# Performance work log

Measured on AMD Instinct MI355X. Metric: run time of the kernel, lower is better.

The kernel has to match this reference:

```python
import jax, jax.numpy as jnp
import numpy as np
from jax.ops import segment_sum

N_PFAS, N_GW, N_SW = 50000, 200000, 20000
D_IN, D_OUT, D_EDGE = 32, 32, 3
E_PG, E_GP, E_PS, E_SP = 2000000, 2000000, 1000000, 1000000


def _params(key):
    ks = jax.random.split(key, 24)
    g = lambda k, s: jax.random.normal(k, s, dtype=jnp.float32) * 0.05
    p = {}
    # SAGEConvWithEdgeAttr for pg (pfas->gw) and gp (gw->pfas)
    for i, rel in enumerate(['pg', 'gp']):
        o = i * 5
        p[f'Wl_{rel}'] = g(ks[o + 0], (D_IN, D_OUT))
        p[f'bl_{rel}'] = g(ks[o + 1], (D_OUT,))
        p[f'Wr_{rel}'] = g(ks[o + 2], (D_IN, D_OUT))
        p[f'We_{rel}'] = g(ks[o + 3], (D_EDGE, D_OUT))
        p[f'be_{rel}'] = g(ks[o + 4], (D_OUT,))
    # plain SAGEConv for ps (pfas->sw) and sp (sw->pfas)
    for i, rel in enumerate(['ps', 'sp']):
        o = 10 + i * 3
        p[f'Wl_{rel}'] = g(ks[o + 0], (D_IN, D_OUT))
        p[f'bl_{rel}'] = g(ks[o + 1], (D_OUT,))
        p[f'Wr_{rel}'] = g(ks[o + 2], (D_IN, D_OUT))
    p['W_out'] = g(ks[16], (D_OUT, 1))
    p['b_out'] = g(ks[17], (1,))
    p['a_prelu'] = jnp.float32(0.25) * jnp.ones((1,), jnp.float32)
    return p


def setup_inputs() -> dict:
    key = jax.random.key(0)
    ks = jax.random.split(key, 16)
    inp = {
        'x_pfas': jax.random.normal(ks[0], (N_PFAS, D_IN), jnp.float32),
        'x_gw': jax.random.normal(ks[1], (N_GW, D_IN), jnp.float32),
        'x_sw': jax.random.normal(ks[2], (N_SW, D_IN), jnp.float32),
        'src_pg': jax.random.randint(ks[3], (E_PG,), 0, N_PFAS),
        'dst_pg': jax.random.randint(ks[4], (E_PG,), 0, N_GW),
        'ea_pg': jax.random.uniform(ks[5], (E_PG, D_EDGE), jnp.float32),
        'src_gp': jax.random.randint(ks[6], (E_GP,), 0, N_GW),
        'dst_gp': jax.random.randint(ks[7], (E_GP,), 0, N_PFAS),
        'ea_gp': jax.random.uniform(ks[8], (E_GP, D_EDGE), jnp.float32),
        'src_ps': jax.random.randint(ks[9], (E_PS,), 0, N_PFAS),
        'dst_ps': jax.random.randint(ks[10], (E_PS,), 0, N_SW),
        'src_sp': jax.random.randint(ks[11], (E_SP,), 0, N_SW),
        'dst_sp': jax.random.randint(ks[12], (E_SP,), 0, N_PFAS),
    }
    inp.update(_params(ks[13]))
    return inp


def _sage(x_src, x_dst, src, dst, Wl, bl, Wr, n_dst):
    # PyG SAGEConv: lin_l(mean_aggr(x_j)) + lin_r(x_dst); lin_r has no bias
    msg = x_src[src]                                   # [E, D_IN]
    s = segment_sum(msg, dst, num_segments=n_dst)      # [n_dst, D_IN]
    cnt = segment_sum(jnp.ones((src.shape[0],), x_src.dtype), dst, num_segments=n_dst)
    mean = s / jnp.maximum(cnt, 1.0)[:, None]
    return mean @ Wl + bl + x_dst @ Wr


def _edge_scatter_set(dst, ea_t, n_dst):
    # matches torch zeros.scatter_(0, col, edge_attr_transformed): overwrite at dst
    return jnp.zeros((n_dst, ea_t.shape[1]), ea_t.dtype).at[dst].set(ea_t)


def reference(x_pfas, x_gw, x_sw,
              src_pg, dst_pg, ea_pg,
              src_gp, dst_gp, ea_gp,
              src_ps, dst_ps, src_sp, dst_sp,
              Wl_pg, bl_pg, Wr_pg, We_pg, be_pg,
              Wl_gp, bl_gp, Wr_gp, We_gp, be_gp,
              Wl_ps, bl_ps, Wr_ps,
              Wl_sp, bl_sp, Wr_sp,
              W_out, b_out, a_prelu):
    # pfas -> gw (edge attrs)
    out_gw = _sage(x_pfas, x_gw, src_pg, dst_pg, Wl_pg, bl_pg, Wr_pg, N_GW)
    out_gw = out_gw + _edge_scatter_set(dst_pg, ea_pg @ We_pg + be_pg, N_GW)
    # gw -> pfas (edge attrs)
    out_pf1 = _sage(x_gw, x_pfas, src_gp, dst_gp, Wl_gp, bl_gp, Wr_gp, N_PFAS)
    out_pf1 = out_pf1 + _edge_scatter_set(dst_gp, ea_gp @ We_gp + be_gp, N_PFAS)
    # sw -> pfas (plain SAGE)
    out_pf2 = _sage(x_sw, x_pfas, src_sp, dst_sp, Wl_sp, bl_sp, Wr_sp, N_PFAS)
    # pfas -> sw (plain SAGE)
    out_sw = _sage(x_pfas, x_sw, src_ps, dst_ps, Wl_ps, bl_ps, Wr_ps, N_SW)
    # HeteroConv aggr='sum' over relations with same dst type, then relu
    h_pfas = jax.nn.relu(out_pf1 + out_pf2)
    h_gw = jax.nn.relu(out_gw)
    h_sw = jax.nn.relu(out_sw)
    # final linear + PReLU on gw_wells
    y = h_gw @ W_out + b_out                           # [N_GW, 1]
    y = jnp.where(y >= 0, y, a_prelu * y)
    return h_pfas, y, h_sw
```

## Files before the change

kernel.cpp:

```cpp
#include <hip/hip_runtime.h>

typedef unsigned int u32;

#define NPFAS 50000
#define NGW   200000
#define NSW   20000
#define D     32
#define EPG   2000000
#define EGP   2000000
#define EPS   1000000
#define ESP   1000000

#define NB_PG 782
#define NB_GP 782
#define NB_SP 391
#define NB_PS 313
#define CAP_PG 2880
#define CAP_GP 2880
#define CAP_SP 2880
#define CAP_PS 3584
#define SORT_MAX 3584
#define EIDM 0x1FFFFFu

#define ZGCUR    0
#define MAXE_PG  2304
#define MAXE_GP  202304
#define S_PG     252304
#define S_GP     6652304
#define S_SP     8252304
#define S_PS     9852304
#define CNT_PG   10492304
#define CNT_GP   10692304
#define CNT_SP   10742304
#define CNT_PS   10792304
#define REG_PG   10812304
#define REG_GP   13064464
#define REG_SP   15316624
#define REG_PS   16442704

__device__ __forceinline__ void part4(
    const int* __restrict__ src, const int* __restrict__ dst,
    int e0, int e1, int nb, int cp, int cf, int pshift, int bbits, int roundSz,
    bool useEid,
    u32* __restrict__ region, int cap, int* __restrict__ gcur,
    u32* binData, u32* binCnt)
{
    u32 dlm = (1u << bbits) - 1u;
    for (int b = threadIdx.x; b < nb; b += 256) binCnt[b] = 0;
    __syncthreads();
    for (int base = e0; base < e1; base += roundSz) {
        int rend = base + roundSz; if (rend > e1) rend = e1;
        for (int e = base + (int)threadIdx.x; e < rend; e += 256) {
            int d = dst[e];
            int bk = d >> bbits;
            u32 payload = useEid ? (u32)e : (u32)src[e];
            u32 w0 = payload | (((u32)d & dlm) << pshift);
            u32 pos = atomicAdd(&binCnt[bk], 1u);
            if ((int)pos < cp) {
                binData[bk * cp + (int)pos] = w0;
            } else {
                int g = atomicAdd(&gcur[bk], 1);
                if (g < cap) region[(size_t)bk * cap + g] = w0;
            }
        }
        __syncthreads();
        bool last = (base + roundSz >= e1);
        for (int b = threadIdx.x; b < nb; b += 256) {
            int c = (int)binCnt[b];
            if (c > cp) c = cp;
            if (c >= cf || (last && c > 0)) {
                int g = atomicAdd(&gcur[b], c);
                int lim = cap - g; if (lim < 0) lim = 0; if (c > lim) c = lim;
                u32* dp = region + ((size_t)b * cap + g);
                for (int i = 0; i < c; i++) dp[i] = binData[b * cp + i];
                binCnt[b] = 0;
            }
        }
        __syncthreads();
    }
}

__global__ __launch_bounds__(256) void partition_all(
    const int* __restrict__ dst_pg,
    const int* __restrict__ dst_gp,
    const int* __restrict__ src_sp, const int* __restrict__ dst_sp,
    const int* __restrict__ src_ps, const int* __restrict__ dst_ps,
    int* __restrict__ wsi)
{
    __shared__ u32 binData[6256];
    __shared__ u32 binCnt[782];
    u32* ws = (u32*)wsi;
    int b = blockIdx.x;
    if (b < 160) {
        int e0 = b * (EPG / 160);
        part4(nullptr, dst_pg, e0, e0 + EPG / 160, NB_PG, 8, 4, 21, 8, 1024, true,
              ws + REG_PG, CAP_PG, wsi + ZGCUR + 0, binData, binCnt);
    } else if (b < 320) {
        int bb = b - 160;
        int e0 = bb * (EGP / 160);
        part4(nullptr, dst_gp, e0, e0 + EGP / 160, NB_GP, 8, 4, 21, 6, 1024, true,
              ws + REG_GP, CAP_GP, wsi + ZGCUR + 782, binData, binCnt);
    } else if (b < 416) {
        int bb = b - 320;
        int e0 = (int)(((long long)bb * ESP) / 96);
        int e1 = (int)(((long long)(bb + 1) * ESP) / 96);
        part4(src_sp, dst_sp, e0, e1, NB_SP, 16, 8, 15, 7, 1024, false,
              ws + REG_SP, CAP_SP, wsi + ZGCUR + 1564, binData, binCnt);
    } else {
        int bb = b - 416;
        int e0 = (int)(((long long)bb * EPS) / 96);
        int e1 = (int)(((long long)(bb + 1) * EPS) / 96);
        part4(src_ps, dst_ps, e0, e1, NB_PS, 16, 8, 16, 6, 1024, false,
              ws + REG_PS, CAP_PS, wsi + ZGCUR + 1955, binData, binCnt);
    }
}

__global__ __launch_bounds__(256) void sort_agg(
    const float* __restrict__ x_pfas, const float* __restrict__ x_gw,
    const float* __restrict__ x_sw,
    const int* __restrict__ src_pg, const int* __restrict__ src_gp,
    int* __restrict__ wsi)
{
    __shared__ u32 sortedS[SORT_MAX];
    __shared__ int histS[256];
    __shared__ int startS[256];
    __shared__ int cursorS[256];
    __shared__ int mxS[256];
    __shared__ int wsum[4];

    float* wsf = (float*)wsi;
    u32* wsu = (u32*)wsi;
    int tid = threadIdx.x;
    int bid = blockIdx.x;

    const float* x; const u32* reg; const int* srcArr; int gi, cap, pshift, nbDst, dbase, ndst;
    u32 smask; bool useEid; float* sOut; float* cntOut; int* mxOut;

    if (bid < NB_PG) {
        x = x_pfas; reg = wsu + REG_PG + (size_t)bid * CAP_PG; gi = ZGCUR + bid;
        cap = CAP_PG; pshift = 21; smask = 0; useEid = true; srcArr = src_pg;
        nbDst = 256; dbase = bid << 8; ndst = NGW;
        sOut = wsf + S_PG; cntOut = wsf + CNT_PG; mxOut = wsi + MAXE_PG;
    } else if (bid < NB_PG + NB_GP) {
        int b = bid - NB_PG;
        x = x_gw; reg = wsu + REG_GP + (size_t)b * CAP_GP; gi = ZGCUR + 782 + b;
        cap = CAP_GP; pshift = 21; smask = 0; useEid = true; srcArr = src_gp;
        nbDst = 64; dbase = b << 6; ndst = NPFAS;
        sOut = wsf + S_GP; cntOut = wsf + CNT_GP; mxOut = wsi + MAXE_GP;
    } else if (bid < NB_PG + NB_GP + NB_SP) {
        int b = bid - NB_PG - NB_GP;
        x = x_sw; reg = wsu + REG_SP + (size_t)b * CAP_SP; gi = ZGCUR + 1564 + b;
        cap = CAP_SP; pshift = 15; smask = 0x7FFFu; useEid = false; srcArr = nullptr;
        nbDst = 128; dbase = b << 7; ndst = NPFAS;
        sOut = wsf + S_SP; cntOut = wsf + CNT_SP; mxOut = nullptr;
    } else {
        int b = bid - NB_PG - NB_GP - NB_SP;
        x = x_pfas; reg = wsu + REG_PS + (size_t)b * CAP_PS; gi = ZGCUR + 1955 + b;
        cap = CAP_PS; pshift = 16; smask = 0xFFFFu; useEid = false; srcArr = nullptr;
        nbDst = 64; dbase = b << 6; ndst = NSW;
        sOut = wsf + S_PS; cntOut = wsf + CNT_PS; mxOut = nullptr;
    }

    int nEnt = wsi[gi]; if (nEnt > cap) nEnt = cap;

    histS[tid] = 0;
    mxS[tid] = -1;
    __syncthreads();

    for (int i = tid; i < nEnt; i += 256) {
        u32 w0 = reg[i];
        int dl = (int)((w0 >> pshift) & 255u);
        atomicAdd(&histS[dl], 1);
        if (useEid) atomicMax(&mxS[dl], (int)(w0 & EIDM));
    }
    __syncthreads();

    {
        int v = histS[tid];
        int lane = tid & 63, w = tid >> 6;
        int incl = v;
#pragma unroll
        for (int off = 1; off < 64; off <<= 1) {
            int t = __shfl_up(incl, off);
            if (lane >= off) incl += t;
        }
        if (lane == 63) wsum[w] = incl;
        startS[tid] = incl - v;
    }
    __syncthreads();
    {
        int w = tid >> 6;
        int off = 0;
        for (int k = 0; k < w; k++) off += wsum[k];
        int st = startS[tid] + off;
        startS[tid] = st;
        cursorS[tid] = st;
    }
    __syncthreads();

    for (int i = tid; i < nEnt; i += 256) {
        u32 w0 = reg[i];
        int dl = (int)((w0 >> pshift) & 255u);
        int pos = atomicAdd(&cursorS[dl], 1);
        u32 sv = useEid ? (u32)srcArr[(int)(w0 & EIDM)] : (w0 & smask);
        if (pos < SORT_MAX) sortedS[pos] = sv;
    }
    __syncthreads();

    int wv = tid >> 6, lane = tid & 63, half = lane >> 5, f = lane & 31;
    for (int q = wv; q < nbDst; q += 4) {
        int dn = dbase + q;
        if (dn >= ndst) continue;
        int deg = histS[q];
        int p0 = startS[q];
        float a = 0.f;
        int i = half;
        for (; i + 6 < deg; i += 8) {
            int s0 = (int)sortedS[p0 + i];
            int s1 = (int)sortedS[p0 + i + 2];
            int s2 = (int)sortedS[p0 + i + 4];
            int s3 = (int)sortedS[p0 + i + 6];
            float v0 = x[(size_t)s0 * D + f];
            float v1 = x[(size_t)s1 * D + f];
            float v2 = x[(size_t)s2 * D + f];
            float v3 = x[(size_t)s3 * D + f];
            a += (v0 + v1) + (v2 + v3);
        }
        for (; i < deg; i += 2) a += x[(size_t)sortedS[p0 + i] * D + f];
        a += __shfl_xor(a, 32);
        if (half == 0) sOut[(size_t)dn * D + f] = a;
        if (lane == 0) {
            cntOut[dn] = (float)deg;
            if (useEid) mxOut[dn] = mxS[q];
        }
    }
}

__global__ __launch_bounds__(256) void finalize_gw(
    const float* __restrict__ s, const float* __restrict__ cntF,
    const int* __restrict__ maxe,
    const float* __restrict__ x_gw,
    const float* __restrict__ ea,
    const float* __restrict__ Wl, const float* __restrict__ bl,
    const float* __restrict__ Wr, const float* __restrict__ We,
    const float* __restrict__ be,
    const float* __restrict__ W_out, const float* __restrict__ b_out,
    const float* __restrict__ a_prelu,
    float* __restrict__ y_out)
{
    __shared__ __align__(16) float WlT[D * D];
    __shared__ __align__(16) float WrT[D * D];
    __shared__ float WeT[3 * D];
    __shared__ float blS[D], beS[D], WoS[D];
    for (int i = threadIdx.x; i < D * D; i += blockDim.x) {
        int k = i / D, j = i % D;
        WlT[j * D + k] = Wl[i];
        WrT[j * D + k] = Wr[i];
    }
    for (int i = threadIdx.x; i < 3 * D; i += blockDim.x) {
        int k = i / D, j = i % D;
        WeT[j * 3 + k] = We[i];
    }
    if (threadIdx.x < D) {
        blS[threadIdx.x] = bl[threadIdx.x];
        beS[threadIdx.x] = be[threadIdx.x];
        WoS[threadIdx.x] = W_out[threadIdx.x];
    }
    __syncthreads();

    int n = blockIdx.x * blockDim.x + threadIdx.x;
    if (n >= NGW) return;

    float mean[D], xd[D];
    float inv = 1.0f / fmaxf(cntF[n], 1.0f);
    const float4* sp = (const float4*)(s + (size_t)n * D);
    const float4* xp = (const float4*)(x_gw + (size_t)n * D);
#pragma unroll
    for (int q = 0; q < D / 4; q++) {
        float4 sv = sp[q];
        mean[4*q+0] = sv.x * inv; mean[4*q+1] = sv.y * inv;
        mean[4*q+2] = sv.z * inv; mean[4*q+3] = sv.w * inv;
        float4 xv = xp[q];
        xd[4*q+0] = xv.x; xd[4*q+1] = xv.y; xd[4*q+2] = xv.z; xd[4*q+3] = xv.w;
    }
    int me = maxe[n];
    bool he = (me >= 0);
    float e0 = 0.f, e1 = 0.f, e2 = 0.f;
    if (he) {
        e0 = ea[(size_t)me * 3 + 0];
        e1 = ea[(size_t)me * 3 + 1];
        e2 = ea[(size_t)me * 3 + 2];
    }
    float yacc = 0.f;
    for (int j = 0; j < D; j++) {
        float o = blS[j] + (he ? beS[j] : 0.0f);
        const float4* wl4 = (const float4*)(WlT + j * D);
        const float4* wr4 = (const float4*)(WrT + j * D);
#pragma unroll
        for (int q = 0; q < D / 4; q++) {
            float4 wl = wl4[q], wr = wr4[q];
            o += mean[4*q+0]*wl.x + mean[4*q+1]*wl.y + mean[4*q+2]*wl.z + mean[4*q+3]*wl.w;
            o += xd[4*q+0]*wr.x + xd[4*q+1]*wr.y + xd[4*q+2]*wr.z + xd[4*q+3]*wr.w;
        }
        if (he) o += e0*WeT[j*3+0] + e1*WeT[j*3+1] + e2*WeT[j*3+2];
        float h = fmaxf(o, 0.0f);
        yacc += h * WoS[j];
    }
    float y = yacc + b_out[0];
    float ap = a_prelu[0];
    y_out[n] = (y >= 0.f) ? y : ap * y;
}

__global__ __launch_bounds__(256) void finalize_pfas(
    const float* __restrict__ s_gp, const float* __restrict__ cnt_gp,
    const int* __restrict__ maxe_gp,
    const float* __restrict__ s_sp, const float* __restrict__ cnt_sp,
    const float* __restrict__ x_pfas,
    const float* __restrict__ ea,
    const float* __restrict__ Wl_gp, const float* __restrict__ bl_gp,
    const float* __restrict__ Wr_gp, const float* __restrict__ We_gp,
    const float* __restrict__ be_gp,
    const float* __restrict__ Wl_sp, const float* __restrict__ bl_sp,
    const float* __restrict__ Wr_sp,
    float* __restrict__ h_out)
{
    __shared__ __align__(16) float WlgT[D * D];
    __shared__ __align__(16) float WlsT[D * D];
    __shared__ __align__(16) float WrcT[D * D];
    __shared__ float WeT[3 * D];
    __shared__ float blc[D], beS[D];
    for (int i = threadIdx.x; i < D * D; i += blockDim.x) {
        int k = i / D, j = i % D;
        WlgT[j * D + k] = Wl_gp[i];
        WlsT[j * D + k] = Wl_sp[i];
        WrcT[j * D + k] = Wr_gp[i] + Wr_sp[i];
    }
    for (int i = threadIdx.x; i < 3 * D; i += blockDim.x) {
        int k = i / D, j = i % D;
        WeT[j * 3 + k] = We_gp[i];
    }
    if (threadIdx.x < D) {
        blc[threadIdx.x] = bl_gp[threadIdx.x] + bl_sp[threadIdx.x];
        beS[threadIdx.x] = be_gp[threadIdx.x];
    }
    __syncthreads();

    int n = blockIdx.x * blockDim.x + threadIdx.x;
    if (n >= NPFAS) return;

    float mg[D], ms[D], xd[D];
    float invg = 1.0f / fmaxf(cnt_gp[n], 1.0f);
    float invs = 1.0f / fmaxf(cnt_sp[n], 1.0f);
    const float4* gp4 = (const float4*)(s_gp + (size_t)n * D);
    const float4* sp4 = (const float4*)(s_sp + (size_t)n * D);
    const float4* xp4 = (const float4*)(x_pfas + (size_t)n * D);
#pragma unroll
    for (int q = 0; q < D / 4; q++) {
        float4 a = gp4[q];
        mg[4*q+0] = a.x * invg; mg[4*q+1] = a.y * invg; mg[4*q+2] = a.z * invg; mg[4*q+3] = a.w * invg;
        float4 b = sp4[q];
        ms[4*q+0] = b.x * invs; ms[4*q+1] = b.y * invs; ms[4*q+2] = b.z * invs; ms[4*q+3] = b.w * invs;
        float4 c = xp4[q];
        xd[4*q+0] = c.x; xd[4*q+1] = c.y; xd[4*q+2] = c.z; xd[4*q+3] = c.w;
    }
    int me = maxe_gp[n];
    bool he = (me >= 0);
    float e0 = 0.f, e1 = 0.f, e2 = 0.f;
    if (he) {
        e0 = ea[(size_t)me * 3 + 0];
        e1 = ea[(size_t)me * 3 + 1];
        e2 = ea[(size_t)me * 3 + 2];
    }
    float* out = h_out + (size_t)n * D;
    for (int j = 0; j < D; j++) {
        float o = blc[j] + (he ? beS[j] : 0.0f);
        const float4* wg4 = (const float4*)(WlgT + j * D);
        const float4* ws4 = (const float4*)(WlsT + j * D);
        const float4* wc4 = (const float4*)(WrcT + j * D);
#pragma unroll
        for (int q = 0; q < D / 4; q++) {
            float4 wg = wg4[q], wsv = ws4[q], wc = wc4[q];
            o += mg[4*q+0]*wg.x + mg[4*q+1]*wg.y + mg[4*q+2]*wg.z + mg[4*q+3]*wg.w;
            o += ms[4*q+0]*wsv.x + ms[4*q+1]*wsv.y + ms[4*q+2]*wsv.z + ms[4*q+3]*wsv.w;
            o += xd[4*q+0]*wc.x + xd[4*q+1]*wc.y + xd[4*q+2]*wc.z + xd[4*q+3]*wc.w;
        }
        if (he) o += e0*WeT[j*3+0] + e1*WeT[j*3+1] + e2*WeT[j*3+2];
        out[j] = fmaxf(o, 0.0f);
    }
}

__global__ __launch_bounds__(256) void finalize_sw(
    const float* __restrict__ s, const float* __restrict__ cntF,
    const float* __restrict__ x_sw,
    const float* __restrict__ Wl, const float* __restrict__ bl,
    const float* __restrict__ Wr,
    float* __restrict__ h_out)
{
    __shared__ __align__(16) float WlT[D * D];
    __shared__ __align__(16) float WrT[D * D];
    __shared__ float blS[D];
    for (int i = threadIdx.x; i < D * D; i += blockDim.x) {
        int k = i / D, j = i % D;
        WlT[j * D + k] = Wl[i];
        WrT[j * D + k] = Wr[i];
    }
    if (threadIdx.x < D) blS[threadIdx.x] = bl[threadIdx.x];
    __syncthreads();

    int n = blockIdx.x * blockDim.x + threadIdx.x;
    if (n >= NSW) return;

    float mean[D], xd[D];
    float inv = 1.0f / fmaxf(cntF[n], 1.0f);
    const float4* sp = (const float4*)(s + (size_t)n * D);
    const float4* xp = (const float4*)(x_sw + (size_t)n * D);
#pragma unroll
    for (int q = 0; q < D / 4; q++) {
        float4 sv = sp[q];
        mean[4*q+0] = sv.x * inv; mean[4*q+1] = sv.y * inv;
        mean[4*q+2] = sv.z * inv; mean[4*q+3] = sv.w * inv;
        float4 xv = xp[q];
        xd[4*q+0] = xv.x; xd[4*q+1] = xv.y; xd[4*q+2] = xv.z; xd[4*q+3] = xv.w;
    }
    float* out = h_out + (size_t)n * D;
    for (int j = 0; j < D; j++) {
        float o = blS[j];
        const float4* wl4 = (const float4*)(WlT + j * D);
        const float4* wr4 = (const float4*)(WrT + j * D);
#pragma unroll
        for (int q = 0; q < D / 4; q++) {
            float4 wl = wl4[q], wr = wr4[q];
            o += mean[4*q+0]*wl.x + mean[4*q+1]*wl.y + mean[4*q+2]*wl.z + mean[4*q+3]*wl.w;
            o += xd[4*q+0]*wr.x + xd[4*q+1]*wr.y + xd[4*q+2]*wr.z + xd[4*q+3]*wr.w;
        }
        out[j] = fmaxf(o, 0.0f);
    }
}

extern "C" void kernel_launch(void* const* d_in, const int* in_sizes, int n_in,
                              void* d_out, int out_size, void* d_ws, size_t ws_size,
                              hipStream_t stream) {
    (void)in_sizes; (void)n_in; (void)out_size; (void)ws_size;
    const float* x_pfas = (const float*)d_in[0];
    const float* x_gw   = (const float*)d_in[1];
    const float* x_sw   = (const float*)d_in[2];
    const int*   src_pg = (const int*)d_in[3];
    const int*   dst_pg = (const int*)d_in[4];
    const float* ea_pg  = (const float*)d_in[5];
    const int*   src_gp = (const int*)d_in[6];
    const int*   dst_gp = (const int*)d_in[7];
    const float* ea_gp  = (const float*)d_in[8];
    const int*   src_ps = (const int*)d_in[9];
    const int*   dst_ps = (const int*)d_in[10];
    const int*   src_sp = (const int*)d_in[11];
    const int*   dst_sp = (const int*)d_in[12];
    const float* Wl_pg = (const float*)d_in[13];
    const float* bl_pg = (const float*)d_in[14];
    const float* Wr_pg = (const float*)d_in[15];
    const float* We_pg = (const float*)d_in[16];
    const float* be_pg = (const float*)d_in[17];
    const float* Wl_gp = (const float*)d_in[18];
    const float* bl_gp = (const float*)d_in[19];
    const float* Wr_gp = (const float*)d_in[20];
    const float* We_gp = (const float*)d_in[21];
    const float* be_gp = (const float*)d_in[22];
    const float* Wl_ps = (const float*)d_in[23];
    const float* bl_ps = (const float*)d_in[24];
    const float* Wr_ps = (const float*)d_in[25];
    const float* Wl_sp = (const float*)d_in[26];
    const float* bl_sp = (const float*)d_in[27];
    const float* Wr_sp = (const float*)d_in[28];
    const float* W_out = (const float*)d_in[29];
    const float* b_out = (const float*)d_in[30];
    const float* a_pre = (const float*)d_in[31];

    int*   wsi = (int*)d_ws;
    float* wsf = (float*)d_ws;

    hipMemsetAsync(wsi + ZGCUR, 0, 2304 * sizeof(int), stream);

    partition_all<<<512, 256, 0, stream>>>(dst_pg, dst_gp,
                                           src_sp, dst_sp, src_ps, dst_ps, wsi);

    sort_agg<<<NB_PG + NB_GP + NB_SP + NB_PS, 256, 0, stream>>>(
        x_pfas, x_gw, x_sw, src_pg, src_gp, wsi);

    float* out    = (float*)d_out;
    float* h_pfas = out;
    float* y_out  = out + 1600000;
    float* h_sw   = out + 1800000;

    finalize_pfas<<<(NPFAS + 255) / 256, 256, 0, stream>>>(
        wsf + S_GP, wsf + CNT_GP, wsi + MAXE_GP, wsf + S_SP, wsf + CNT_SP,
        x_pfas, ea_gp,
        Wl_gp, bl_gp, Wr_gp, We_gp, be_gp,
        Wl_sp, bl_sp, Wr_sp, h_pfas);

    finalize_gw<<<(NGW + 255) / 256, 256, 0, stream>>>(
        wsf + S_PG, wsf + CNT_PG, wsi + MAXE_PG, x_gw, ea_pg,
        Wl_pg, bl_pg, Wr_pg, We_pg, be_pg,
        W_out, b_out, a_pre, y_out);

    finalize_sw<<<(NSW + 255) / 256, 256, 0, stream>>>(
        wsf + S_PS, wsf + CNT_PS, x_sw, Wl_ps, bl_ps, Wr_ps, h_sw);
}
```

Measured before the change: 511.1 us.

## Gather pfas/gw features from fp16 copies and enlarge partition bin buffers

Adds a kernel that converts x_pfas and x_gw to half precision in workspace, and the neighbor-sum gather in sort_agg reads these fp16 copies to halve gather bytes per edge. The partition kernel also doubles the per-bin shared staging capacity and flush thresholds, so global flushes are fewer and larger. The cost is an extra conversion pass over about 8M floats, fp16 rounding in the aggregated features, and more shared memory per block, which may lower occupancy.

```diff
diff --git a/kernel.cpp b/kernel.cpp
--- a/kernel.cpp
+++ b/kernel.cpp
@@ -1,4 +1,5 @@
 #include <hip/hip_runtime.h>
+#include <hip/hip_fp16.h>
 
 typedef unsigned int u32;
 
@@ -37,6 +38,28 @@
 #define REG_GP   13064464
 #define REG_SP   15316624
 #define REG_PS   16442704
+#define XH_PFAS  17564496
+#define XH_GW    18364496
+
+__global__ __launch_bounds__(256) void convert_x(
+    const float* __restrict__ xp, const float* __restrict__ xg, int* __restrict__ wsi)
+{
+    int i = blockIdx.x * 256 + threadIdx.x;
+    __half2* hp = (__half2*)(wsi + XH_PFAS);
+    __half2* hg = (__half2*)(wsi + XH_GW);
+    const float2* fp = (const float2*)xp;
+    const float2* fg = (const float2*)xg;
+    if (i < NPFAS * D / 2) {
+        float2 v = fp[i];
+        hp[i] = __floats2half2_rn(v.x, v.y);
+        return;
+    }
+    i -= NPFAS * D / 2;
+    if (i < NGW * D / 2) {
+        float2 v = fg[i];
+        hg[i] = __floats2half2_rn(v.x, v.y);
+    }
+}
 
 __device__ __forceinline__ void part4(
     const int* __restrict__ src, const int* __restrict__ dst,
@@ -87,36 +110,35 @@
     const int* __restrict__ src_ps, const int* __restrict__ dst_ps,
     int* __restrict__ wsi)
 {
-    __shared__ u32 binData[6256];
+    __shared__ u32 binData[12512];
     __shared__ u32 binCnt[782];
     u32* ws = (u32*)wsi;
     int b = blockIdx.x;
     if (b < 160) {
         int e0 = b * (EPG / 160);
-        part4(nullptr, dst_pg, e0, e0 + EPG / 160, NB_PG, 8, 4, 21, 8, 1024, true,
+        part4(nullptr, dst_pg, e0, e0 + EPG / 160, NB_PG, 16, 10, 21, 8, 1024, true,
               ws + REG_PG, CAP_PG, wsi + ZGCUR + 0, binData, binCnt);
     } else if (b < 320) {
         int bb = b - 160;
         int e0 = bb * (EGP / 160);
-        part4(nullptr, dst_gp, e0, e0 + EGP / 160, NB_GP, 8, 4, 21, 6, 1024, true,
+        part4(nullptr, dst_gp, e0, e0 + EGP / 160, NB_GP, 16, 10, 21, 6, 1024, true,
               ws + REG_GP, CAP_GP, wsi + ZGCUR + 782, binData, binCnt);
     } else if (b < 416) {
         int bb = b - 320;
         int e0 = (int)(((long long)bb * ESP) / 96);
         int e1 = (int)(((long long)(bb + 1) * ESP) / 96);
-        part4(src_sp, dst_sp, e0, e1, NB_SP, 16, 8, 15, 7, 1024, false,
+        part4(src_sp, dst_sp, e0, e1, NB_SP, 32, 24, 15, 7, 1024, false,
               ws + REG_SP, CAP_SP, wsi + ZGCUR + 1564, binData, binCnt);
     } else {
         int bb = b - 416;
         int e0 = (int)(((long long)bb * EPS) / 96);
         int e1 = (int)(((long long)(bb + 1) * EPS) / 96);
-        part4(src_ps, dst_ps, e0, e1, NB_PS, 16, 8, 16, 6, 1024, false,
+        part4(src_ps, dst_ps, e0, e1, NB_PS, 32, 24, 16, 6, 1024, false,
               ws + REG_PS, CAP_PS, wsi + ZGCUR + 1955, binData, binCnt);
     }
 }
 
 __global__ __launch_bounds__(256) void sort_agg(
-    const float* __restrict__ x_pfas, const float* __restrict__ x_gw,
     const float* __restrict__ x_sw,
     const int* __restrict__ src_pg, const int* __restrict__ src_gp,
     int* __restrict__ wsi)
@@ -133,29 +155,34 @@
     int tid = threadIdx.x;
     int bid = blockIdx.x;
 
-    const float* x; const u32* reg; const int* srcArr; int gi, cap, pshift, nbDst, dbase, ndst;
+    const __half* xh = nullptr; const float* xf = nullptr;
+    const u32* reg; const int* srcArr; int gi, cap, pshift, nbDst, dbase, ndst;
     u32 smask; bool useEid; float* sOut; float* cntOut; int* mxOut;
 
     if (bid < NB_PG) {
-        x = x_pfas; reg = wsu + REG_PG + (size_t)bid * CAP_PG; gi = ZGCUR + bid;
+        xh = (const __half*)(wsi + XH_PFAS);
+        reg = wsu + REG_PG + (size_t)bid * CAP_PG; gi = ZGCUR + bid;
         cap = CAP_PG; pshift = 21; smask = 0; useEid = true; srcArr = src_pg;
         nbDst = 256; dbase = bid << 8; ndst = NGW;
         sOut = wsf + S_PG; cntOut = wsf + CNT_PG; mxOut = wsi + MAXE_PG;
     } else if (bid < NB_PG + NB_GP) {
         int b = bid - NB_PG;
-        x = x_gw; reg = wsu + REG_GP + (size_t)b * CAP_GP; gi = ZGCUR + 782 + b;
+        xh = (const __half*)(wsi + XH_GW);
+        reg = wsu + REG_GP + (size_t)b * CAP_GP; gi = ZGCUR + 782 + b;
         cap = CAP_GP; pshift = 21; smask = 0; useEid = true; srcArr = src_gp;
         nbDst = 64; dbase = b << 6; ndst = NPFAS;
         sOut = wsf + S_GP; cntOut = wsf + CNT_GP; mxOut = wsi + MAXE_GP;
     } else if (bid < NB_PG + NB_GP + NB_SP) {
         int b = bid - NB_PG - NB_GP;
-        x = x_sw; reg = wsu + REG_SP + (size_t)b * CAP_SP; gi = ZGCUR + 1564 + b;
+        xf = x_sw;
+        reg = wsu + REG_SP + (size_t)b * CAP_SP; gi = ZGCUR + 1564 + b;
         cap = CAP_SP; pshift = 15; smask = 0x7FFFu; useEid = false; srcArr = nullptr;
         nbDst = 128; dbase = b << 7; ndst = NPFAS;
         sOut = wsf + S_SP; cntOut = wsf + CNT_SP; mxOut = nullptr;
     } else {
         int b = bid - NB_PG - NB_GP - NB_SP;
-        x = x_pfas; reg = wsu + REG_PS + (size_t)b * CAP_PS; gi = ZGCUR + 1955 + b;
+        xh = (const __half*)(wsi + XH_PFAS);
+        reg = wsu + REG_PS + (size_t)b * CAP_PS; gi = ZGCUR + 1955 + b;
         cap = CAP_PS; pshift = 16; smask = 0xFFFFu; useEid = false; srcArr = nullptr;
         nbDst = 64; dbase = b << 6; ndst = NSW;
         sOut = wsf + S_PS; cntOut = wsf + CNT_PS; mxOut = nullptr;
@@ -215,18 +242,33 @@
         int p0 = startS[q];
         float a = 0.f;
         int i = half;
-        for (; i + 6 < deg; i += 8) {
-            int s0 = (int)sortedS[p0 + i];
-            int s1 = (int)sortedS[p0 + i + 2];
-            int s2 = (int)sortedS[p0 + i + 4];
-            int s3 = (int)sortedS[p0 + i + 6];
-            float v0 = x[(size_t)s0 * D + f];
-            float v1 = x[(size_t)s1 * D + f];
-            float v2 = x[(size_t)s2 * D + f];
-            float v3 = x[(size_t)s3 * D + f];
-            a += (v0 + v1) + (v2 + v3);
-        }
-        for (; i < deg; i += 2) a += x[(size_t)sortedS[p0 + i] * D + f];
+        if (xh) {
+            for (; i + 6 < deg; i += 8) {
+                int s0 = (int)sortedS[p0 + i];
+                int s1 = (int)sortedS[p0 + i + 2];
+                int s2 = (int)sortedS[p0 + i + 4];
+                int s3 = (int)sortedS[p0 + i + 6];
+                float v0 = __half2float(xh[(size_t)s0 * D + f]);
+                float v1 = __half2float(xh[(size_t)s1 * D + f]);
+                float v2 = __half2float(xh[(size_t)s2 * D + f]);
+                float v3 = __half2float(xh[(size_t)s3 * D + f]);
+                a += (v0 + v1) + (v2 + v3);
+            }
+            for (; i < deg; i += 2) a += __half2float(xh[(size_t)sortedS[p0 + i] * D + f]);
+        } else {
+            for (; i + 6 < deg; i += 8) {
+                int s0 = (int)sortedS[p0 + i];
+                int s1 = (int)sortedS[p0 + i + 2];
+                int s2 = (int)sortedS[p0 + i + 4];
+                int s3 = (int)sortedS[p0 + i + 6];
+                float v0 = xf[(size_t)s0 * D + f];
+                float v1 = xf[(size_t)s1 * D + f];
+                float v2 = xf[(size_t)s2 * D + f];
+                float v3 = xf[(size_t)s3 * D + f];
+                a += (v0 + v1) + (v2 + v3);
+            }
+            for (; i < deg; i += 2) a += xf[(size_t)sortedS[p0 + i] * D + f];
+        }
         a += __shfl_xor(a, 32);
         if (half == 0) sOut[(size_t)dn * D + f] = a;
         if (lane == 0) {
@@ -479,11 +521,14 @@
 
     hipMemsetAsync(wsi + ZGCUR, 0, 2304 * sizeof(int), stream);
 
+    convert_x<<<(NPFAS * D / 2 + NGW * D / 2 + 255) / 256, 256, 0, stream>>>(
+        x_pfas, x_gw, wsi);
+
     partition_all<<<512, 256, 0, stream>>>(dst_pg, dst_gp,
                                            src_sp, dst_sp, src_ps, dst_ps, wsi);
 
     sort_agg<<<NB_PG + NB_GP + NB_SP + NB_PS, 256, 0, stream>>>(
-        x_pfas, x_gw, x_sw, src_pg, src_gp, wsi);
+        x_sw, src_pg, src_gp, wsi);
 
     float* out    = (float*)d_out;
     float* h_pfas = out;
```

Result: faster. 493.4 us (-3.5%).
